# Kernel tuning notes

Measured on AMD Instinct MI355X. Metric: run time of the kernel, lower is better.

The kernel has to match this reference:

```python
import jax, jax.numpy as jnp
import numpy as np

D_MODEL = 1024
HEADS = 16
D_K = D_MODEL // HEADS
D_FF = 4096
B, S = 8, 1024
EPS = 1e-5
NEG = -1e9


def layer_norm(x, g, b):
    mu = jnp.mean(x, axis=-1, keepdims=True)
    var = jnp.var(x, axis=-1, keepdims=True)
    return (x - mu) * jax.lax.rsqrt(var + EPS) * g + b


def setup_inputs() -> dict:
    key = jax.random.key(0)
    ks = jax.random.split(key, 10)
    sc = lambda d: 1.0 / np.sqrt(d)
    return {
        "x": jax.random.normal(ks[0], (B, S, D_MODEL), jnp.float32),
        "mask": jnp.ones((B, 1, 1, S), jnp.int32),
        "wq": jax.random.normal(ks[1], (D_MODEL, D_MODEL), jnp.float32) * sc(D_MODEL),
        "bq": jnp.zeros((D_MODEL,), jnp.float32),
        "wk": jax.random.normal(ks[2], (D_MODEL, D_MODEL), jnp.float32) * sc(D_MODEL),
        "bk": jnp.zeros((D_MODEL,), jnp.float32),
        "wv": jax.random.normal(ks[3], (D_MODEL, D_MODEL), jnp.float32) * sc(D_MODEL),
        "bv": jnp.zeros((D_MODEL,), jnp.float32),
        "wo": jax.random.normal(ks[4], (D_MODEL, D_MODEL), jnp.float32) * sc(D_MODEL),
        "bo": jnp.zeros((D_MODEL,), jnp.float32),
        "w1": jax.random.normal(ks[5], (D_MODEL, D_FF), jnp.float32) * sc(D_MODEL),
        "b1": jnp.zeros((D_FF,), jnp.float32),
        "w2": jax.random.normal(ks[6], (D_FF, D_MODEL), jnp.float32) * sc(D_FF),
        "b2": jnp.zeros((D_MODEL,), jnp.float32),
        "ln1_g": jnp.ones((D_MODEL,), jnp.float32),
        "ln1_b": jnp.zeros((D_MODEL,), jnp.float32),
        "ln2_g": jnp.ones((D_MODEL,), jnp.float32),
        "ln2_b": jnp.zeros((D_MODEL,), jnp.float32),
    }


def reference(x, mask, wq, bq, wk, bk, wv, bv, wo, bo, w1, b1, w2, b2,
              ln1_g, ln1_b, ln2_g, ln2_b):
    b, s, d = x.shape

    # --- self-attention sublayer with residual + LN (pre-norm, dropout=0) ---
    h = layer_norm(x, ln1_g, ln1_b)
    q = (h @ wq + bq).reshape(b, s, HEADS, D_K).transpose(0, 2, 1, 3)  # [b,h,s,dk]
    k = (h @ wk + bk).reshape(b, s, HEADS, D_K).transpose(0, 2, 1, 3)
    v = (h @ wv + bv).reshape(b, s, HEADS, D_K).transpose(0, 2, 1, 3)

    scores = jnp.einsum("bhqd,bhkd->bhqk", q, k) / np.sqrt(D_K)  # [b,h,s,s]
    scores = jnp.where(mask == 0, NEG, scores)
    attn = jax.nn.softmax(scores, axis=-1)
    ctx = jnp.einsum("bhqk,bhkd->bhqd", attn, v)
    ctx = ctx.transpose(0, 2, 1, 3).reshape(b, s, d)
    x = x + (ctx @ wo + bo)

    # --- feed-forward sublayer with residual + LN ---
    h2 = layer_norm(x, ln2_g, ln2_b)
    ff = jax.nn.relu(h2 @ w1 + b1) @ w2 + b2
    return x + ff
```

## Files before the change

kernel.cpp:

```cpp
#include <hip/hip_runtime.h>
#include <hip/hip_bf16.h>

typedef __attribute__((ext_vector_type(8))) __bf16 bf16x8;
typedef __attribute__((ext_vector_type(4))) __bf16 bf16x4;
typedef __attribute__((ext_vector_type(4))) float  f32x4;

__device__ __forceinline__ void gload_lds16(const __bf16* g, __bf16* l) {
    __builtin_amdgcn_global_load_lds(
        (const __attribute__((address_space(1))) void*)g,
        (__attribute__((address_space(3))) void*)l, 16, 0, 0);
}

__global__ void transpose_convert(const float* __restrict__ in,
                                  __bf16* __restrict__ out, int K, int N) {
    __shared__ float t[32][33];
    const int nb = blockIdx.x * 32, kb = blockIdx.y * 32;
    const int tx = threadIdx.x & 31, ty = threadIdx.x >> 5;
#pragma unroll
    for (int i = 0; i < 32; i += 8)
        t[ty + i][tx] = in[(size_t)(kb + ty + i) * N + nb + tx];
    __syncthreads();
#pragma unroll
    for (int i = 0; i < 32; i += 8)
        out[(size_t)(nb + ty + i) * K + kb + tx] = (__bf16)t[tx][ty + i];
}

__global__ void concat3(const float* __restrict__ a, const float* __restrict__ b,
                        const float* __restrict__ c, float* __restrict__ o, int n) {
    int i = blockIdx.x * 256 + threadIdx.x;
    if (i < n) { o[i] = a[i]; o[n + i] = b[i]; o[2 * n + i] = c[i]; }
}

__global__ __launch_bounds__(256) void ln_to_bf16(const float* __restrict__ x,
                                                  const float* __restrict__ g,
                                                  const float* __restrict__ bb,
                                                  __bf16* __restrict__ out) {
    const int row = blockIdx.x, t = threadIdx.x;
    const float4 v = ((const float4*)(x + (size_t)row * 1024))[t];
    float s  = v.x + v.y + v.z + v.w;
    float ss = v.x * v.x + v.y * v.y + v.z * v.z + v.w * v.w;
#pragma unroll
    for (int off = 32; off; off >>= 1) {
        s  += __shfl_down(s, off);
        ss += __shfl_down(ss, off);
    }
    __shared__ float ps[4], pss[4];
    if ((t & 63) == 0) { ps[t >> 6] = s; pss[t >> 6] = ss; }
    __syncthreads();
    s  = ps[0] + ps[1] + ps[2] + ps[3];
    ss = pss[0] + pss[1] + pss[2] + pss[3];
    const float mu   = s * (1.0f / 1024.0f);
    const float var  = ss * (1.0f / 1024.0f) - mu * mu;
    const float rinv = rsqrtf(var + 1e-5f);
    const float4 gv = ((const float4*)g)[t];
    const float4 bv = ((const float4*)bb)[t];
    bf16x4 o;
    o[0] = (__bf16)((v.x - mu) * rinv * gv.x + bv.x);
    o[1] = (__bf16)((v.y - mu) * rinv * gv.y + bv.y);
    o[2] = (__bf16)((v.z - mu) * rinv * gv.z + bv.z);
    o[3] = (__bf16)((v.w - mu) * rinv * gv.w + bv.w);
    *(bf16x4*)(out + (size_t)row * 1024 + 4 * t) = o;
}

template <int MODE>
__global__ __launch_bounds__(512, 2) void gemm256(const __bf16* __restrict__ A,
                                                  const __bf16* __restrict__ BT,
                                                  const float* __restrict__ bias,
                                                  __bf16* __restrict__ outp,
                                                  __bf16* __restrict__ vTout,
                                                  int M, int N, int K, int NMB) {
    __shared__ __align__(16) __bf16 lds[65536];
    const int nwg = gridDim.x;
    const int bid = blockIdx.x;
    const int wgid = (bid & 7) * (nwg >> 3) + (bid >> 3);
    const int bm = (wgid % NMB) * 256, bn = (wgid / NMB) * 256;
    const int tid = threadIdx.x, l = tid & 63, w = tid >> 6;
    const int wm = (w >> 2) * 128, wn = (w & 3) * 64;
    const int lg = l >> 4, lm = l & 15;
    const int NT = K >> 6;

    const __bf16* gsrc[4];
    int ldst[4];
#pragma unroll
    for (int j = 0; j < 4; ++j) {
        const unsigned X = (unsigned)(((j & 1) << 13) + (w << 10) + l * 16);
        const unsigned L = X ^ (((X >> 7) & 7u) << 4);
        const int row = L >> 6, col = (L & 63) >> 1;
        gsrc[j] = (j < 2 ? A + (size_t)(bm + row) * K : BT + (size_t)(bn + row) * K) + col;
        ldst[j] = ((j < 2 ? 0 : 16384) + ((j & 1) << 13) + (w << 10)) >> 1;
    }
    int aoff[2][4], boff[4];
#pragma unroll
    for (int mh = 0; mh < 2; ++mh)
#pragma unroll
        for (int fr = 0; fr < 4; ++fr) {
            const unsigned Lb = (unsigned)(wm + mh * 64 + fr * 16 + lm) * 64 + lg * 16;
            aoff[mh][fr] = (int)(Lb ^ (((Lb >> 7) & 7u) << 4)) >> 1;
        }
#pragma unroll
    for (int n = 0; n < 4; ++n) {
        const unsigned Lb = (unsigned)(wn + n * 16 + lm) * 64 + lg * 16;
        boff[n] = (int)(16384u + (Lb ^ (((Lb >> 7) & 7u) << 4))) >> 1;
    }

    f32x4 acc[8][4];
#pragma unroll
    for (int m = 0; m < 8; ++m)
#pragma unroll
        for (int n = 0; n < 4; ++n) acc[m][n] = f32x4{0.f, 0.f, 0.f, 0.f};

#define ISSUE_SUB(u)                                                          \
    do {                                                                      \
        __bf16* sbp = lds + (((u) & 3) << 14);                                \
        const int go = (u) << 5;                                              \
        _Pragma("unroll")                                                     \
        for (int j = 0; j < 4; ++j) gload_lds16(gsrc[j] + go, sbp + ldst[j]); \
    } while (0)

#define MFMA16(MH, BREG)                                                      \
    do {                                                                      \
        __builtin_amdgcn_s_setprio(1);                                        \
        _Pragma("unroll")                                                     \
        for (int i = 0; i < 4; ++i)                                           \
            _Pragma("unroll")                                                 \
            for (int n = 0; n < 4; ++n)                                       \
                acc[(MH)*4 + i][n] = __builtin_amdgcn_mfma_f32_16x16x32_bf16( \
                    af[i], BREG[n], acc[(MH)*4 + i][n], 0, 0, 0);             \
        __builtin_amdgcn_s_setprio(0);                                        \
    } while (0)

    ISSUE_SUB(0); ISSUE_SUB(1); ISSUE_SUB(2); ISSUE_SUB(3);
    asm volatile("s_waitcnt vmcnt(8)" ::: "memory");
    __builtin_amdgcn_s_barrier();

    for (int t = 0; t < NT; ++t) {
        const int sa = ((2 * t) & 3) << 14, sb = ((2 * t + 1) & 3) << 14;
        bf16x8 af[4], b0[4], b1[4];
#pragma unroll
        for (int fr = 0; fr < 4; ++fr) af[fr] = *(const bf16x8*)(lds + sa + aoff[0][fr]);
#pragma unroll
        for (int n = 0; n < 4; ++n) b0[n] = *(const bf16x8*)(lds + sa + boff[n]);
        asm volatile("" ::: "memory");
        __builtin_amdgcn_s_barrier();
        __builtin_amdgcn_sched_barrier(0);
        MFMA16(0, b0);
        __builtin_amdgcn_sched_barrier(0);
        __builtin_amdgcn_s_barrier();
#pragma unroll
        for (int fr = 0; fr < 4; ++fr) af[fr] = *(const bf16x8*)(lds + sa + aoff[1][fr]);
        asm volatile("" ::: "memory");
        __builtin_amdgcn_s_barrier();
        __builtin_amdgcn_sched_barrier(0);
        MFMA16(1, b0);
        __builtin_amdgcn_sched_barrier(0);
        __builtin_amdgcn_s_barrier();
        if (t < NT - 2) ISSUE_SUB(2 * t + 4);
#pragma unroll
        for (int fr = 0; fr < 4; ++fr) af[fr] = *(const bf16x8*)(lds + sb + aoff[0][fr]);
#pragma unroll
        for (int n = 0; n < 4; ++n) b1[n] = *(const bf16x8*)(lds + sb + boff[n]);
        asm volatile("" ::: "memory");
        __builtin_amdgcn_s_barrier();
        __builtin_amdgcn_sched_barrier(0);
        MFMA16(0, b1);
        __builtin_amdgcn_sched_barrier(0);
        __builtin_amdgcn_s_barrier();
#pragma unroll
        for (int fr = 0; fr < 4; ++fr) af[fr] = *(const bf16x8*)(lds + sb + aoff[1][fr]);
        asm volatile("" ::: "memory");
        __builtin_amdgcn_s_barrier();
        __builtin_amdgcn_sched_barrier(0);
        MFMA16(1, b1);
        __builtin_amdgcn_sched_barrier(0);
        __builtin_amdgcn_s_barrier();
        if (t < NT - 2) {
            ISSUE_SUB(2 * t + 5);
            asm volatile("s_waitcnt vmcnt(8)" ::: "memory");
        } else if (t == NT - 2) {
            asm volatile("s_waitcnt vmcnt(0)" ::: "memory");
        }
        __builtin_amdgcn_s_barrier();
    }
#undef ISSUE_SUB
#undef MFMA16

    const int ldc = (MODE == 4) ? 2048 : N;
    const bool isQ = (MODE == 4) && (bn < 1024);
#pragma unroll
    for (int m = 0; m < 8; ++m) {
        const int row = bm + wm + (m >> 2) * 64 + (m & 3) * 16 + lg * 4;
#pragma unroll
        for (int n = 0; n < 4; ++n) {
            const int col = bn + wn + n * 16 + lm;
            const float bvv = bias[col];
            if (MODE == 4 && bn >= 2048) {
                bf16x4 o;
#pragma unroll
                for (int r = 0; r < 4; ++r) o[r] = (__bf16)(acc[m][n][r] + bvv);
                *(bf16x4*)(vTout + (size_t)((row >> 10) * 1024 + (col - 2048)) * 1024 +
                           (row & 1023)) = o;
            } else {
#pragma unroll
                for (int r = 0; r < 4; ++r) {
                    float v = acc[m][n][r] + bvv;
                    if (isQ) v *= 0.125f;
                    outp[(size_t)(row + r) * ldc + col] =
                        (MODE == 1) ? (__bf16)fmaxf(v, 0.f) : (__bf16)v;
                }
            }
        }
    }
}

__global__ __launch_bounds__(512, 2) void gemm256x128(const __bf16* __restrict__ A,
                                                      const __bf16* __restrict__ BT,
                                                      const float* __restrict__ bias,
                                                      const float* __restrict__ resid,
                                                      float* __restrict__ outp,
                                                      int M, int N, int K, int NMB) {
    __shared__ __align__(16) __bf16 lds[49152];
    const int nwg = gridDim.x;
    const int bid = blockIdx.x;
    const int wgid = (bid & 7) * (nwg >> 3) + (bid >> 3);
    const int bm = (wgid % NMB) * 256, bn = (wgid / NMB) * 128;
    const int tid = threadIdx.x, l = tid & 63, w = tid >> 6;
    const int wm = (w >> 1) * 64, wn = (w & 1) * 64;
    const int lg = l >> 4, lm = l & 15;
    const int NT = K >> 6;

    const __bf16* gsrc[3];
    int ldst[3];
#pragma unroll
    for (int j = 0; j < 3; ++j) {
        const unsigned X = (unsigned)((j == 1 ? 8192 : 0) + tid * 16);
        const unsigned L = X ^ (((X >> 7) & 7u) << 4);
        const int row = L >> 6, col = (L & 63) >> 1;
        gsrc[j] = (j < 2 ? A + (size_t)(bm + row) * K : BT + (size_t)(bn + row) * K) + col;
        ldst[j] = ((j < 2 ? (j << 13) : 16384) + (w << 10)) >> 1;
    }
    int aoff[2][2], boff[4];
#pragma unroll
    for (int mh = 0; mh < 2; ++mh)
#pragma unroll
        for (int fr = 0; fr < 2; ++fr) {
            const unsigned Lb = (unsigned)(wm + mh * 32 + fr * 16 + lm) * 64 + lg * 16;
            aoff[mh][fr] = (int)(Lb ^ (((Lb >> 7) & 7u) << 4)) >> 1;
        }
#pragma unroll
    for (int n = 0; n < 4; ++n) {
        const unsigned Lb = (unsigned)(wn + n * 16 + lm) * 64 + lg * 16;
        boff[n] = (int)(16384u + (Lb ^ (((Lb >> 7) & 7u) << 4))) >> 1;
    }

    f32x4 acc[4][4];
#pragma unroll
    for (int m = 0; m < 4; ++m)
#pragma unroll
        for (int n = 0; n < 4; ++n) acc[m][n] = f32x4{0.f, 0.f, 0.f, 0.f};

#define ISSUE_SUB(u)                                                          \
    do {                                                                      \
        __bf16* sbp = lds + ((u) & 3) * 12288;                                \
        const int go = (u) << 5;                                              \
        _Pragma("unroll")                                                     \
        for (int j = 0; j < 3; ++j) gload_lds16(gsrc[j] + go, sbp + ldst[j]); \
    } while (0)

#define MFMA8(MH, BREG)                                                       \
    do {                                                                      \
        __builtin_amdgcn_s_setprio(1);                                        \
        _Pragma("unroll")                                                     \
        for (int i = 0; i < 2; ++i)                                           \
            _Pragma("unroll")                                                 \
            for (int n = 0; n < 4; ++n)                                       \
                acc[(MH)*2 + i][n] = __builtin_amdgcn_mfma_f32_16x16x32_bf16( \
                    af[i], BREG[n], acc[(MH)*2 + i][n], 0, 0, 0);             \
        __builtin_amdgcn_s_setprio(0);                                        \
    } while (0)

    ISSUE_SUB(0); ISSUE_SUB(1); ISSUE_SUB(2); ISSUE_SUB(3);
    asm volatile("s_waitcnt vmcnt(6)" ::: "memory");
    __builtin_amdgcn_s_barrier();

    for (int t = 0; t < NT; ++t) {
        const int sa = ((2 * t) & 3) * 12288, sb = ((2 * t + 1) & 3) * 12288;
        bf16x8 af[2], b0[4], b1[4];
#pragma unroll
        for (int fr = 0; fr < 2; ++fr) af[fr] = *(const bf16x8*)(lds + sa + aoff[0][fr]);
#pragma unroll
        for (int n = 0; n < 4; ++n) b0[n] = *(const bf16x8*)(lds + sa + boff[n]);
        asm volatile("" ::: "memory");
        __builtin_amdgcn_s_barrier();
        __builtin_amdgcn_sched_barrier(0);
        MFMA8(0, b0);
        __builtin_amdgcn_sched_barrier(0);
        __builtin_amdgcn_s_barrier();
#pragma unroll
        for (int fr = 0; fr < 2; ++fr) af[fr] = *(const bf16x8*)(lds + sa + aoff[1][fr]);
        asm volatile("" ::: "memory");
        __builtin_amdgcn_s_barrier();
        __builtin_amdgcn_sched_barrier(0);
        MFMA8(1, b0);
        __builtin_amdgcn_sched_barrier(0);
        __builtin_amdgcn_s_barrier();
        if (t < NT - 2) ISSUE_SUB(2 * t + 4);
#pragma unroll
        for (int fr = 0; fr < 2; ++fr) af[fr] = *(const bf16x8*)(lds + sb + aoff[0][fr]);
#pragma unroll
        for (int n = 0; n < 4; ++n) b1[n] = *(const bf16x8*)(lds + sb + boff[n]);
        asm volatile("" ::: "memory");
        __builtin_amdgcn_s_barrier();
        __builtin_amdgcn_sched_barrier(0);
        MFMA8(0, b1);
        __builtin_amdgcn_sched_barrier(0);
        __builtin_amdgcn_s_barrier();
#pragma unroll
        for (int fr = 0; fr < 2; ++fr) af[fr] = *(const bf16x8*)(lds + sb + aoff[1][fr]);
        asm volatile("" ::: "memory");
        __builtin_amdgcn_s_barrier();
        __builtin_amdgcn_sched_barrier(0);
        MFMA8(1, b1);
        __builtin_amdgcn_sched_barrier(0);
        __builtin_amdgcn_s_barrier();
        if (t < NT - 2) {
            ISSUE_SUB(2 * t + 5);
            asm volatile("s_waitcnt vmcnt(6)" ::: "memory");
        } else if (t == NT - 2) {
            asm volatile("s_waitcnt vmcnt(0)" ::: "memory");
        }
        __builtin_amdgcn_s_barrier();
    }
#undef ISSUE_SUB
#undef MFMA8

#pragma unroll
    for (int m = 0; m < 4; ++m) {
        const int row = bm + wm + m * 16 + lg * 4;
#pragma unroll
        for (int n = 0; n < 4; ++n) {
            const int col = bn + wn + n * 16 + lm;
            const float bvv = bias[col];
#pragma unroll
            for (int r = 0; r < 4; ++r) {
                const size_t idx = (size_t)(row + r) * N + col;
                outp[idx] = resid[idx] + acc[m][n][r] + bvv;
            }
        }
    }
}

__global__ __launch_bounds__(256) void attn_kernel(const __bf16* __restrict__ qk,
                                                   const __bf16* __restrict__ vT,
                                                   const int* __restrict__ mask,
                                                   __bf16* __restrict__ ctx) {
    const int qt = blockIdx.x, h = blockIdx.y, b = blockIdx.z;
    const int tid = threadIdx.x, w = tid >> 6, l = tid & 63;
    const int lg = l >> 4, lm = l & 15;

    __shared__ __align__(16) __bf16 Ks[64][76];
    __shared__ __align__(16) __bf16 Vt[64][76];
    __shared__ __align__(16) __bf16 Ps[4][16][76];
    __shared__ int smask[64];

    const int qrow = qt * 64 + w * 16 + lm;
    const __bf16* qp = qk + (size_t)(b * 1024 + qrow) * 2048 + h * 64 + lg * 8;
    bf16x8 aq[2];
    aq[0] = *(const bf16x8*)qp;
    aq[1] = *(const bf16x8*)(qp + 32);

    float mrun = -1e30f, lsum = 0.f;
    f32x4 oacc[4];
#pragma unroll
    for (int n = 0; n < 4; ++n) oacc[n] = f32x4{0.f, 0.f, 0.f, 0.f};

    for (int kt = 0; kt < 16; ++kt) {
#pragma unroll
        for (int it = 0; it < 2; ++it) {
            const int c = tid + it * 256;
            const int r = c >> 3, cc = (c & 7) * 8;
            *(uint4*)&Ks[r][cc] =
                *(const uint4*)&qk[(size_t)(b * 1024 + kt * 64 + r) * 2048 + 1024 + h * 64 + cc];
            *(uint4*)&Vt[r][cc] =
                *(const uint4*)&vT[(size_t)(b * 1024 + h * 64 + r) * 1024 + kt * 64 + cc];
        }
        if (tid < 64) smask[tid] = mask[b * 1024 + kt * 64 + tid];
        __syncthreads();

        f32x4 sacc[4];
#pragma unroll
        for (int n = 0; n < 4; ++n) {
            sacc[n] = f32x4{0.f, 0.f, 0.f, 0.f};
#pragma unroll
            for (int kk = 0; kk < 2; ++kk) {
                bf16x8 bk = *(const bf16x8*)&Ks[n * 16 + lm][lg * 8 + kk * 32];
                sacc[n] = __builtin_amdgcn_mfma_f32_16x16x32_bf16(bk, aq[kk], sacc[n], 0, 0, 0);
            }
        }
        float p[4][4], mloc = -3e38f;
#pragma unroll
        for (int n = 0; n < 4; ++n) {
            const int4 mk = *(const int4*)&smask[n * 16 + lg * 4];
            const int mka[4] = {mk.x, mk.y, mk.z, mk.w};
#pragma unroll
            for (int r = 0; r < 4; ++r) {
                const float sv = (mka[r] == 0) ? -1e9f : sacc[n][r];
                p[n][r] = sv;
                mloc = fmaxf(mloc, sv);
            }
        }
        mloc = fmaxf(mloc, __shfl_xor(mloc, 16));
        mloc = fmaxf(mloc, __shfl_xor(mloc, 32));
        const float pm = fmaxf(mrun, mloc);
        if (!__all(pm - mrun <= 8.f)) {
            const float sc = __expf(mrun - pm);
            mrun = pm;
            lsum *= sc;
            float scr[4];
#pragma unroll
            for (int r = 0; r < 4; ++r) scr[r] = __shfl(sc, lg * 4 + r);
#pragma unroll
            for (int n = 0; n < 4; ++n)
#pragma unroll
                for (int r = 0; r < 4; ++r) oacc[n][r] *= scr[r];
        }
        float rs = 0.f;
#pragma unroll
        for (int n = 0; n < 4; ++n)
#pragma unroll
            for (int r = 0; r < 4; ++r) {
                p[n][r] = __expf(p[n][r] - mrun);
                rs += p[n][r];
            }
        rs += __shfl_xor(rs, 16);
        rs += __shfl_xor(rs, 32);
        lsum += rs;
#pragma unroll
        for (int n = 0; n < 4; ++n) {
            bf16x4 pb;
#pragma unroll
            for (int r = 0; r < 4; ++r) pb[r] = (__bf16)p[n][r];
            *(bf16x4*)&Ps[w][lm][n * 16 + lg * 4] = pb;
        }
        bf16x8 ap[2];
        ap[0] = *(const bf16x8*)&Ps[w][lm][lg * 8];
        ap[1] = *(const bf16x8*)&Ps[w][lm][lg * 8 + 32];
#pragma unroll
        for (int n = 0; n < 4; ++n)
#pragma unroll
            for (int kk = 0; kk < 2; ++kk) {
                bf16x8 bv = *(const bf16x8*)&Vt[n * 16 + lm][lg * 8 + kk * 32];
                oacc[n] = __builtin_amdgcn_mfma_f32_16x16x32_bf16(ap[kk], bv, oacc[n], 0, 0, 0);
            }
        __syncthreads();
    }
    float lsr[4];
#pragma unroll
    for (int r = 0; r < 4; ++r) lsr[r] = __shfl(lsum, lg * 4 + r);
#pragma unroll
    for (int n = 0; n < 4; ++n)
#pragma unroll
        for (int r = 0; r < 4; ++r) {
            const float val = oacc[n][r] / lsr[r];
            const int row = qt * 64 + w * 16 + lg * 4 + r;
            ctx[(size_t)(b * 1024 + row) * 1024 + h * 64 + n * 16 + lm] = (__bf16)val;
        }
}

extern "C" void kernel_launch(void* const* d_in, const int* in_sizes, int n_in,
                              void* d_out, int out_size, void* d_ws, size_t ws_size,
                              hipStream_t stream) {
    const float* x    = (const float*)d_in[0];
    const int*   mask = (const int*)d_in[1];
    const float* wq   = (const float*)d_in[2];
    const float* bq   = (const float*)d_in[3];
    const float* wk   = (const float*)d_in[4];
    const float* bk   = (const float*)d_in[5];
    const float* wv   = (const float*)d_in[6];
    const float* bv   = (const float*)d_in[7];
    const float* wo   = (const float*)d_in[8];
    const float* bo   = (const float*)d_in[9];
    const float* w1   = (const float*)d_in[10];
    const float* b1   = (const float*)d_in[11];
    const float* w2   = (const float*)d_in[12];
    const float* b2   = (const float*)d_in[13];
    const float* ln1g = (const float*)d_in[14];
    const float* ln1b = (const float*)d_in[15];
    const float* ln2g = (const float*)d_in[16];
    const float* ln2b = (const float*)d_in[17];
    float* out = (float*)d_out;
    char* ws = (char*)d_ws;

    __bf16* wqkvT = (__bf16*)(ws + 0);
    __bf16* woT   = (__bf16*)(ws + 6291456);
    __bf16* w1T   = (__bf16*)(ws + 8388608);
    __bf16* w2T   = (__bf16*)(ws + 16777216);
    float*  bqkv  = (float*)(ws + 25165824);
    __bf16* hb    = (__bf16*)(ws + 25178112);
    __bf16* qkb   = (__bf16*)(ws + 41955328);
    __bf16* vTb   = (__bf16*)(ws + 75509760);
    __bf16* ctxb  = (__bf16*)(ws + 92286976);
    __bf16* ff1b  = qkb;

    transpose_convert<<<dim3(32, 32),  256, 0, stream>>>(wq, wqkvT,               1024, 1024);
    transpose_convert<<<dim3(32, 32),  256, 0, stream>>>(wk, wqkvT + 1024 * 1024, 1024, 1024);
    transpose_convert<<<dim3(32, 32),  256, 0, stream>>>(wv, wqkvT + 2048 * 1024, 1024, 1024);
    transpose_convert<<<dim3(32, 32),  256, 0, stream>>>(wo, woT,                 1024, 1024);
    transpose_convert<<<dim3(128, 32), 256, 0, stream>>>(w1, w1T,                 1024, 4096);
    transpose_convert<<<dim3(32, 128), 256, 0, stream>>>(w2, w2T,                 4096, 1024);
    concat3<<<4, 256, 0, stream>>>(bq, bk, bv, bqkv, 1024);

    ln_to_bf16<<<8192, 256, 0, stream>>>(x, ln1g, ln1b, hb);
    gemm256<4><<<384, 512, 0, stream>>>(hb, wqkvT, bqkv, qkb, vTb, 8192, 3072, 1024, 32);
    attn_kernel<<<dim3(16, 16, 8), 256, 0, stream>>>(qkb, vTb, mask, ctxb);
    gemm256x128<<<256, 512, 0, stream>>>(ctxb, woT, bo, x, out, 8192, 1024, 1024, 32);
    ln_to_bf16<<<8192, 256, 0, stream>>>(out, ln2g, ln2b, hb);
    gemm256<1><<<512, 512, 0, stream>>>(hb, w1T, b1, ff1b, nullptr, 8192, 4096, 1024, 32);
    gemm256x128<<<256, 512, 0, stream>>>(ff1b, w2T, b2, out, out, 8192, 1024, 4096, 32);
}
```

Before: 404.5 us.

## Merge weight transposes, add 128x256 QKV GEMM, double-buffer attention with exp2

The six weight transpose launches become one combined kernel. The QKV projection moves to a new 128x256-tile GEMM with 768 workgroups, which gives better occupancy and wave balance than 384 workgroups of 256x256. The attention kernel now uses 512 threads over 128 query rows and double-buffers its K/V tiles through registers so loads overlap compute. It reads the mask straight from global memory and uses exp2 with log2e folded into the Q scale. The wider rescale threshold in exp2 units and the mask read pattern change numerics and memory traffic slightly.

```diff
diff --git a/kernel.cpp b/kernel.cpp
--- a/kernel.cpp
+++ b/kernel.cpp
@@ -11,10 +11,30 @@
         (__attribute__((address_space(3))) void*)l, 16, 0, 0);
 }
 
-__global__ void transpose_convert(const float* __restrict__ in,
-                                  __bf16* __restrict__ out, int K, int N) {
+__global__ __launch_bounds__(256) void transpose_all(
+    const float* __restrict__ wq, const float* __restrict__ wk,
+    const float* __restrict__ wv, const float* __restrict__ wo,
+    const float* __restrict__ w1, const float* __restrict__ w2,
+    __bf16* __restrict__ wqkvT, __bf16* __restrict__ woT,
+    __bf16* __restrict__ w1T, __bf16* __restrict__ w2T) {
     __shared__ float t[32][33];
-    const int nb = blockIdx.x * 32, kb = blockIdx.y * 32;
+    const int bid = blockIdx.x;
+    const float* in; __bf16* out; int K, N, nb, kb;
+    if (bid < 4096) {
+        const int which = bid >> 10, tt = bid & 1023;
+        K = 1024; N = 1024;
+        in  = which == 0 ? wq : which == 1 ? wk : which == 2 ? wv : wo;
+        out = which == 3 ? woT : wqkvT + (size_t)which * 1048576;
+        nb = (tt & 31) * 32; kb = (tt >> 5) * 32;
+    } else if (bid < 8192) {
+        const int tt = bid - 4096;
+        in = w1; out = w1T; K = 1024; N = 4096;
+        nb = (tt & 127) * 32; kb = (tt >> 7) * 32;
+    } else {
+        const int tt = bid - 8192;
+        in = w2; out = w2T; K = 4096; N = 1024;
+        nb = (tt & 31) * 32; kb = (tt >> 5) * 32;
+    }
     const int tx = threadIdx.x & 31, ty = threadIdx.x >> 5;
 #pragma unroll
     for (int i = 0; i < 32; i += 8)
@@ -67,7 +87,6 @@
                                                   const __bf16* __restrict__ BT,
                                                   const float* __restrict__ bias,
                                                   __bf16* __restrict__ outp,
-                                                  __bf16* __restrict__ vTout,
                                                   int M, int N, int K, int NMB) {
     __shared__ __align__(16) __bf16 lds[65536];
     const int nwg = gridDim.x;
@@ -184,8 +203,6 @@
 #undef ISSUE_SUB
 #undef MFMA16
 
-    const int ldc = (MODE == 4) ? 2048 : N;
-    const bool isQ = (MODE == 4) && (bn < 1024);
 #pragma unroll
     for (int m = 0; m < 8; ++m) {
         const int row = bm + wm + (m >> 2) * 64 + (m & 3) * 16 + lg * 4;
@@ -193,20 +210,11 @@
         for (int n = 0; n < 4; ++n) {
             const int col = bn + wn + n * 16 + lm;
             const float bvv = bias[col];
-            if (MODE == 4 && bn >= 2048) {
-                bf16x4 o;
-#pragma unroll
-                for (int r = 0; r < 4; ++r) o[r] = (__bf16)(acc[m][n][r] + bvv);
-                *(bf16x4*)(vTout + (size_t)((row >> 10) * 1024 + (col - 2048)) * 1024 +
-                           (row & 1023)) = o;
-            } else {
-#pragma unroll
-                for (int r = 0; r < 4; ++r) {
-                    float v = acc[m][n][r] + bvv;
-                    if (isQ) v *= 0.125f;
-                    outp[(size_t)(row + r) * ldc + col] =
-                        (MODE == 1) ? (__bf16)fmaxf(v, 0.f) : (__bf16)v;
-                }
+#pragma unroll
+            for (int r = 0; r < 4; ++r) {
+                const float v = acc[m][n][r] + bvv;
+                outp[(size_t)(row + r) * N + col] =
+                    (MODE == 1) ? (__bf16)fmaxf(v, 0.f) : (__bf16)v;
             }
         }
     }
@@ -349,7 +357,154 @@
     }
 }
 
-__global__ __launch_bounds__(256) void attn_kernel(const __bf16* __restrict__ qk,
+__global__ __launch_bounds__(512, 2) void gemm_qkv(const __bf16* __restrict__ A,
+                                                   const __bf16* __restrict__ BT,
+                                                   const float* __restrict__ bias,
+                                                   __bf16* __restrict__ outp,
+                                                   __bf16* __restrict__ vTout,
+                                                   int M, int N, int K, int NMB) {
+    __shared__ __align__(16) __bf16 lds[49152];
+    const int nwg = gridDim.x;
+    const int bid = blockIdx.x;
+    const int wgid = (bid & 7) * (nwg >> 3) + (bid >> 3);
+    const int bm = (wgid % NMB) * 128, bn = (wgid / NMB) * 256;
+    const int tid = threadIdx.x, l = tid & 63, w = tid >> 6;
+    const int wm = (w >> 2) * 64, wn = (w & 3) * 64;
+    const int lg = l >> 4, lm = l & 15;
+    const int NT = K >> 6;
+
+    const __bf16* gsrc[3];
+    int ldst[3];
+#pragma unroll
+    for (int j = 0; j < 3; ++j) {
+        const unsigned X = (unsigned)((j == 0 ? 0 : (j - 1) * 8192) + tid * 16);
+        const unsigned L = X ^ (((X >> 7) & 7u) << 4);
+        const int row = L >> 6, col = (L & 63) >> 1;
+        gsrc[j] = (j == 0 ? A + (size_t)(bm + row) * K : BT + (size_t)(bn + row) * K) + col;
+        ldst[j] = ((j == 0 ? 0 : 8192 + (j - 1) * 8192) + (w << 10)) >> 1;
+    }
+    int aoff[2][2], boff[4];
+#pragma unroll
+    for (int mh = 0; mh < 2; ++mh)
+#pragma unroll
+        for (int fr = 0; fr < 2; ++fr) {
+            const unsigned Lb = (unsigned)(wm + mh * 32 + fr * 16 + lm) * 64 + lg * 16;
+            aoff[mh][fr] = (int)(Lb ^ (((Lb >> 7) & 7u) << 4)) >> 1;
+        }
+#pragma unroll
+    for (int n = 0; n < 4; ++n) {
+        const unsigned Lb = (unsigned)(wn + n * 16 + lm) * 64 + lg * 16;
+        boff[n] = (int)(8192u + (Lb ^ (((Lb >> 7) & 7u) << 4))) >> 1;
+    }
+
+    f32x4 acc[4][4];
+#pragma unroll
+    for (int m = 0; m < 4; ++m)
+#pragma unroll
+        for (int n = 0; n < 4; ++n) acc[m][n] = f32x4{0.f, 0.f, 0.f, 0.f};
+
+#define ISSUE_SUB(u)                                                          \
+    do {                                                                      \
+        __bf16* sbp = lds + ((u) & 3) * 12288;                                \
+        const int go = (u) << 5;                                              \
+        _Pragma("unroll")                                                     \
+        for (int j = 0; j < 3; ++j) gload_lds16(gsrc[j] + go, sbp + ldst[j]); \
+    } while (0)
+
+#define MFMA8(MH, BREG)                                                       \
+    do {                                                                      \
+        __builtin_amdgcn_s_setprio(1);                                        \
+        _Pragma("unroll")                                                     \
+        for (int i = 0; i < 2; ++i)                                           \
+            _Pragma("unroll")                                                 \
+            for (int n = 0; n < 4; ++n)                                       \
+                acc[(MH)*2 + i][n] = __builtin_amdgcn_mfma_f32_16x16x32_bf16( \
+                    af[i], BREG[n], acc[(MH)*2 + i][n], 0, 0, 0);             \
+        __builtin_amdgcn_s_setprio(0);                                        \
+    } while (0)
+
+    ISSUE_SUB(0); ISSUE_SUB(1); ISSUE_SUB(2); ISSUE_SUB(3);
+    asm volatile("s_waitcnt vmcnt(6)" ::: "memory");
+    __builtin_amdgcn_s_barrier();
+
+    for (int t = 0; t < NT; ++t) {
+        const int sa = ((2 * t) & 3) * 12288, sb = ((2 * t + 1) & 3) * 12288;
+        bf16x8 af[2], b0[4], b1[4];
+#pragma unroll
+        for (int fr = 0; fr < 2; ++fr) af[fr] = *(const bf16x8*)(lds + sa + aoff[0][fr]);
+#pragma unroll
+        for (int n = 0; n < 4; ++n) b0[n] = *(const bf16x8*)(lds + sa + boff[n]);
+        asm volatile("" ::: "memory");
+        __builtin_amdgcn_s_barrier();
+        __builtin_amdgcn_sched_barrier(0);
+        MFMA8(0, b0);
+        __builtin_amdgcn_sched_barrier(0);
+        __builtin_amdgcn_s_barrier();
+#pragma unroll
+        for (int fr = 0; fr < 2; ++fr) af[fr] = *(const bf16x8*)(lds + sa + aoff[1][fr]);
+        asm volatile("" ::: "memory");
+        __builtin_amdgcn_s_barrier();
+        __builtin_amdgcn_sched_barrier(0);
+        MFMA8(1, b0);
+        __builtin_amdgcn_sched_barrier(0);
+        __builtin_amdgcn_s_barrier();
+        if (t < NT - 2) ISSUE_SUB(2 * t + 4);
+#pragma unroll
+        for (int fr = 0; fr < 2; ++fr) af[fr] = *(const bf16x8*)(lds + sb + aoff[0][fr]);
+#pragma unroll
+        for (int n = 0; n < 4; ++n) b1[n] = *(const bf16x8*)(lds + sb + boff[n]);
+        asm volatile("" ::: "memory");
+        __builtin_amdgcn_s_barrier();
+        __builtin_amdgcn_sched_barrier(0);
+        MFMA8(0, b1);
+        __builtin_amdgcn_sched_barrier(0);
+        __builtin_amdgcn_s_barrier();
+#pragma unroll
+        for (int fr = 0; fr < 2; ++fr) af[fr] = *(const bf16x8*)(lds + sb + aoff[1][fr]);
+        asm volatile("" ::: "memory");
+        __builtin_amdgcn_s_barrier();
+        __builtin_amdgcn_sched_barrier(0);
+        MFMA8(1, b1);
+        __builtin_amdgcn_sched_barrier(0);
+        __builtin_amdgcn_s_barrier();
+        if (t < NT - 2) {
+            ISSUE_SUB(2 * t + 5);
+            asm volatile("s_waitcnt vmcnt(6)" ::: "memory");
+        } else if (t == NT - 2) {
+            asm volatile("s_waitcnt vmcnt(0)" ::: "memory");
+        }
+        __builtin_amdgcn_s_barrier();
+    }
+#undef ISSUE_SUB
+#undef MFMA8
+
+    const bool isQ = bn < 1024;
+#pragma unroll
+    for (int m = 0; m < 4; ++m) {
+        const int row = bm + wm + m * 16 + lg * 4;
+#pragma unroll
+        for (int n = 0; n < 4; ++n) {
+            const int col = bn + wn + n * 16 + lm;
+            const float bvv = bias[col];
+            if (bn >= 2048) {
+                bf16x4 o;
+#pragma unroll
+                for (int r = 0; r < 4; ++r) o[r] = (__bf16)(acc[m][n][r] + bvv);
+                *(bf16x4*)(vTout + (size_t)((row >> 10) * 1024 + (col - 2048)) * 1024 +
+                           (row & 1023)) = o;
+            } else {
+#pragma unroll
+                for (int r = 0; r < 4; ++r) {
+                    float v = acc[m][n][r] + bvv;
+                    if (isQ) v *= 0.18033688f;
+                    outp[(size_t)(row + r) * 2048 + col] = (__bf16)v;
+                }
+            }
+        }
+    }
+}
+
+__global__ __launch_bounds__(512) void attn_kernel(const __bf16* __restrict__ qk,
                                                    const __bf16* __restrict__ vT,
                                                    const int* __restrict__ mask,
                                                    __bf16* __restrict__ ctx) {
@@ -357,62 +512,69 @@
     const int tid = threadIdx.x, w = tid >> 6, l = tid & 63;
     const int lg = l >> 4, lm = l & 15;
 
-    __shared__ __align__(16) __bf16 Ks[64][76];
-    __shared__ __align__(16) __bf16 Vt[64][76];
-    __shared__ __align__(16) __bf16 Ps[4][16][76];
-    __shared__ int smask[64];
-
-    const int qrow = qt * 64 + w * 16 + lm;
+    __shared__ __align__(16) __bf16 Ks[2][64][76];
+    __shared__ __align__(16) __bf16 Vt[2][64][76];
+    __shared__ __align__(16) __bf16 Ps[8][16][76];
+
+    const int qrow = qt * 128 + w * 16 + lm;
     const __bf16* qp = qk + (size_t)(b * 1024 + qrow) * 2048 + h * 64 + lg * 8;
     bf16x8 aq[2];
     aq[0] = *(const bf16x8*)qp;
     aq[1] = *(const bf16x8*)(qp + 32);
 
+    const int r0 = tid >> 3, cc0 = (tid & 7) * 8;
+    const __bf16* kbase = qk + (size_t)(b * 1024 + r0) * 2048 + 1024 + h * 64 + cc0;
+    const __bf16* vbase = vT + (size_t)(b * 1024 + h * 64 + r0) * 1024 + cc0;
+    uint4 kreg, vreg;
+#define ALOAD(kt)                                                      \
+    do {                                                               \
+        kreg = *(const uint4*)(kbase + (size_t)(kt) * 64 * 2048);      \
+        vreg = *(const uint4*)(vbase + (kt) * 64);                     \
+    } while (0)
+#define AWRITE(bf)                                                     \
+    do {                                                               \
+        *(uint4*)&Ks[bf][r0][cc0] = kreg;                              \
+        *(uint4*)&Vt[bf][r0][cc0] = vreg;                              \
+    } while (0)
+
+    ALOAD(0); AWRITE(0); ALOAD(1);
+    __syncthreads();
+
+    const int* mbase = mask + b * 1024;
     float mrun = -1e30f, lsum = 0.f;
     f32x4 oacc[4];
 #pragma unroll
     for (int n = 0; n < 4; ++n) oacc[n] = f32x4{0.f, 0.f, 0.f, 0.f};
 
     for (int kt = 0; kt < 16; ++kt) {
-#pragma unroll
-        for (int it = 0; it < 2; ++it) {
-            const int c = tid + it * 256;
-            const int r = c >> 3, cc = (c & 7) * 8;
-            *(uint4*)&Ks[r][cc] =
-                *(const uint4*)&qk[(size_t)(b * 1024 + kt * 64 + r) * 2048 + 1024 + h * 64 + cc];
-            *(uint4*)&Vt[r][cc] =
-                *(const uint4*)&vT[(size_t)(b * 1024 + h * 64 + r) * 1024 + kt * 64 + cc];
-        }
-        if (tid < 64) smask[tid] = mask[b * 1024 + kt * 64 + tid];
-        __syncthreads();
-
+        const int cur = kt & 1;
         f32x4 sacc[4];
+        int4 mk4[4];
 #pragma unroll
         for (int n = 0; n < 4; ++n) {
+            mk4[n] = *(const int4*)(mbase + kt * 64 + n * 16 + lg * 4);
             sacc[n] = f32x4{0.f, 0.f, 0.f, 0.f};
 #pragma unroll
             for (int kk = 0; kk < 2; ++kk) {
-                bf16x8 bk = *(const bf16x8*)&Ks[n * 16 + lm][lg * 8 + kk * 32];
+                bf16x8 bk = *(const bf16x8*)&Ks[cur][n * 16 + lm][lg * 8 + kk * 32];
                 sacc[n] = __builtin_amdgcn_mfma_f32_16x16x32_bf16(bk, aq[kk], sacc[n], 0, 0, 0);
             }
         }
-        float p[4][4], mloc = -3e38f;
+        float p[4][4], mn[4];
 #pragma unroll
         for (int n = 0; n < 4; ++n) {
-            const int4 mk = *(const int4*)&smask[n * 16 + lg * 4];
-            const int mka[4] = {mk.x, mk.y, mk.z, mk.w};
-#pragma unroll
-            for (int r = 0; r < 4; ++r) {
-                const float sv = (mka[r] == 0) ? -1e9f : sacc[n][r];
-                p[n][r] = sv;
-                mloc = fmaxf(mloc, sv);
-            }
-        }
+            p[n][0] = mk4[n].x ? sacc[n][0] : -1e9f;
+            p[n][1] = mk4[n].y ? sacc[n][1] : -1e9f;
+            p[n][2] = mk4[n].z ? sacc[n][2] : -1e9f;
+            p[n][3] = mk4[n].w ? sacc[n][3] : -1e9f;
+            mn[n] = fmaxf(fmaxf(p[n][0], p[n][1]), fmaxf(p[n][2], p[n][3]));
+        }
+        float mloc = fmaxf(fmaxf(mn[0], mn[1]), fmaxf(mn[2], mn[3]));
         mloc = fmaxf(mloc, __shfl_xor(mloc, 16));
         mloc = fmaxf(mloc, __shfl_xor(mloc, 32));
         const float pm = fmaxf(mrun, mloc);
-        if (!__all(pm - mrun <= 8.f)) {
-            const float sc = __expf(mrun - pm);
+        if (!__all(pm - mrun <= 11.5f)) {
+            const float sc = exp2f(mrun - pm);
             mrun = pm;
             lsum *= sc;
             float scr[4];
@@ -423,14 +585,14 @@
 #pragma unroll
                 for (int r = 0; r < 4; ++r) oacc[n][r] *= scr[r];
         }
-        float rs = 0.f;
-#pragma unroll
-        for (int n = 0; n < 4; ++n)
-#pragma unroll
-            for (int r = 0; r < 4; ++r) {
-                p[n][r] = __expf(p[n][r] - mrun);
-                rs += p[n][r];
-            }
+        float rsn[4];
+#pragma unroll
+        for (int n = 0; n < 4; ++n) {
+#pragma unroll
+            for (int r = 0; r < 4; ++r) p[n][r] = exp2f(p[n][r] - mrun);
+            rsn[n] = (p[n][0] + p[n][1]) + (p[n][2] + p[n][3]);
+        }
+        float rs = (rsn[0] + rsn[1]) + (rsn[2] + rsn[3]);
         rs += __shfl_xor(rs, 16);
         rs += __shfl_xor(rs, 32);
         lsum += rs;
@@ -448,11 +610,16 @@
         for (int n = 0; n < 4; ++n)
 #pragma unroll
             for (int kk = 0; kk < 2; ++kk) {
-                bf16x8 bv = *(const bf16x8*)&Vt[n * 16 + lm][lg * 8 + kk * 32];
+                bf16x8 bv = *(const bf16x8*)&Vt[cur][n * 16 + lm][lg * 8 + kk * 32];
                 oacc[n] = __builtin_amdgcn_mfma_f32_16x16x32_bf16(ap[kk], bv, oacc[n], 0, 0, 0);
             }
         __syncthreads();
-    }
+        if (kt < 15) AWRITE(cur ^ 1);
+        if (kt < 14) ALOAD(kt + 2);
+        __syncthreads();
+    }
+#undef ALOAD
+#undef AWRITE
     float lsr[4];
 #pragma unroll
     for (int r = 0; r < 4; ++r) lsr[r] = __shfl(lsum, lg * 4 + r);
@@ -461,7 +628,7 @@
 #pragma unroll
         for (int r = 0; r < 4; ++r) {
             const float val = oacc[n][r] / lsr[r];
-            const int row = qt * 64 + w * 16 + lg * 4 + r;
+            const int row = qt * 128 + w * 16 + lg * 4 + r;
             ctx[(size_t)(b * 1024 + row) * 1024 + h * 64 + n * 16 + lm] = (__bf16)val;
         }
 }
@@ -501,19 +668,15 @@
     __bf16* ctxb  = (__bf16*)(ws + 92286976);
     __bf16* ff1b  = qkb;
 
-    transpose_convert<<<dim3(32, 32),  256, 0, stream>>>(wq, wqkvT,               1024, 1024);
-    transpose_convert<<<dim3(32, 32),  256, 0, stream>>>(wk, wqkvT + 1024 * 1024, 1024, 1024);
-    transpose_convert<<<dim3(32, 32),  256, 0, stream>>>(wv, wqkvT + 2048 * 1024, 1024, 1024);
-    transpose_convert<<<dim3(32, 32),  256, 0, stream>>>(wo, woT,                 1024, 1024);
-    transpose_convert<<<dim3(128, 32), 256, 0, stream>>>(w1, w1T,                 1024, 4096);
-    transpose_convert<<<dim3(32, 128), 256, 0, stream>>>(w2, w2T,                 4096, 1024);
+    transpose_all<<<12288, 256, 0, stream>>>(wq, wk, wv, wo, w1, w2,
+                                             wqkvT, woT, w1T, w2T);
     concat3<<<4, 256, 0, stream>>>(bq, bk, bv, bqkv, 1024);
 
     ln_to_bf16<<<8192, 256, 0, stream>>>(x, ln1g, ln1b, hb);
-    gemm256<4><<<384, 512, 0, stream>>>(hb, wqkvT, bqkv, qkb, vTb, 8192, 3072, 1024, 32);
-    attn_kernel<<<dim3(16, 16, 8), 256, 0, stream>>>(qkb, vTb, mask, ctxb);
+    gemm_qkv<<<768, 512, 0, stream>>>(hb, wqkvT, bqkv, qkb, vTb, 8192, 3072, 1024, 64);
+    attn_kernel<<<dim3(8, 16, 8), 512, 0, stream>>>(qkb, vTb, mask, ctxb);
     gemm256x128<<<256, 512, 0, stream>>>(ctxb, woT, bo, x, out, 8192, 1024, 1024, 32);
     ln_to_bf16<<<8192, 256, 0, stream>>>(out, ln2g, ln2b, hb);
-    gemm256<1><<<512, 512, 0, stream>>>(hb, w1T, b1, ff1b, nullptr, 8192, 4096, 1024, 32);
+    gemm256<1><<<512, 512, 0, stream>>>(hb, w1T, b1, ff1b, 8192, 4096, 1024, 32);
     gemm256x128<<<256, 512, 0, stream>>>(ff1b, w2T, b2, out, out, 8192, 1024, 4096, 32);
 }
```

New measurement: 394.6 us. 2.4% less time.
